# Kernel optimization log

Hardware: AMD Instinct MI355X
Metric: run time of the kernel (lower is better)

The kernel has to match this reference:

```python
import jax, jax.numpy as jnp
import numpy as np

NUM_EXPERTS = 32
TOP_K = 8
SELECT_TOP_K = 4
THRESHOLD = 0.5
HIDDEN = 2048
D_FF = 768


def setup_inputs() -> dict:
    key = jax.random.key(0)
    ks = jax.random.split(key, 5)
    hidden_states = jax.random.normal(ks[0], (4, 2048, HIDDEN), dtype=jnp.float32)
    gate_weight = jax.random.normal(ks[1], (NUM_EXPERTS, HIDDEN), dtype=jnp.float32) * 0.02
    gate_up_proj = jax.random.normal(ks[2], (NUM_EXPERTS, 2 * D_FF, HIDDEN), dtype=jnp.float32) * 0.02
    down_proj = jax.random.normal(ks[3], (NUM_EXPERTS, HIDDEN, D_FF), dtype=jnp.float32) * 0.02
    similarity = jax.random.uniform(ks[4], (NUM_EXPERTS, NUM_EXPERTS), dtype=jnp.float32)
    return {
        "hidden_states": hidden_states,
        "gate_weight": gate_weight,
        "gate_up_proj": gate_up_proj,
        "down_proj": down_proj,
        "similarity": similarity,
    }


def _moe_forward(hidden_states, gate_weight, gate_up_proj, down_proj, similarity):
    B, S_len, H = hidden_states.shape
    E, K, Ssel = NUM_EXPERTS, TOP_K, SELECT_TOP_K
    x = hidden_states.reshape(-1, H)  # [T, H]

    # Router: logits -> fp32 softmax -> top-k -> renormalize
    router_logits = x @ gate_weight.T  # [T, E]
    router_probs = jax.nn.softmax(router_logits.astype(jnp.float32), axis=-1).astype(router_logits.dtype)
    router_top_value, router_indices = jax.lax.top_k(router_probs, K)  # [T, K]
    routing_weights = router_top_value / jnp.clip(
        jnp.sum(router_top_value, axis=-1, keepdims=True), 1e-12, None
    )

    # SERE rerouting: map each secondary expert to its most-similar primary expert
    sim = similarity.astype(jnp.float32)
    sim = sim.at[jnp.arange(E), jnp.arange(E)].set(1.0)  # fill_diagonal_(1.0)
    prim = router_indices[:, :Ssel]            # [T, S]
    sec = router_indices[:, Ssel:]             # [T, K-S]
    sim_cand = sim[sec[:, :, None], prim[:, None, :]]        # [T, K-S, S]
    best_sim = jnp.max(sim_cand, axis=-1)                    # [T, K-S]
    best_i = jnp.argmax(sim_cand, axis=-1)                   # [T, K-S]
    prim_rep = jnp.broadcast_to(prim[:, None, :], sim_cand.shape)
    best_primary = jnp.take_along_axis(prim_rep, best_i[..., None], axis=-1)[..., 0]
    new_sec = jnp.where(best_sim < THRESHOLD, sec, best_primary) if THRESHOLD > 0.0 else best_primary
    rerouted_indices = jnp.concatenate([prim, new_sec], axis=1)  # [T, K]

    # Combine weights per (token, expert); duplicate expert slots accumulate (index_add semantics)
    combine = jnp.sum(
        jax.nn.one_hot(rerouted_indices, E, dtype=routing_weights.dtype)
        * routing_weights[..., None],
        axis=1,
    )  # [T, E]

    # Dense masked expert sweep (scan over experts keeps peak memory at one [T, 2*D_FF] buffer)
    def expert_step(y, params):
        wgu, wd, cw = params  # [2F, H], [H, F], [T]
        gu = x @ wgu.T                      # [T, 2F]
        g, u = jnp.split(gu, 2, axis=-1)
        h = jax.nn.silu(g) * u              # SwiGLU
        y = y + (h @ wd.T) * cw[:, None]
        return y, None

    y0 = jnp.zeros_like(x)
    y, _ = jax.lax.scan(expert_step, y0, (gate_up_proj, down_proj, combine.T))
    return y.reshape(B, S_len, H)


def reference(hidden_states, gate_weight, gate_up_proj, down_proj, similarity):
    return _moe_forward(hidden_states, gate_weight, gate_up_proj, down_proj, similarity)
```

## Files before the change

kernel.cpp:

```cpp
#include <hip/hip_runtime.h>
#include <stdint.h>
#include <string.h>

#define NTOK 8192
#define HID 2048
#define NE 32
#define DFF 768
#define NSLOT 65536
#define NB 256
#define MT 256
#define MAX_TILES 288

typedef unsigned short u16;
typedef unsigned int u32;

using f32x4 = __attribute__((ext_vector_type(4))) float;
using bf16x8 = __attribute__((ext_vector_type(8))) short;

static __device__ __forceinline__ u16 f2bf(float f) {
  u32 x = __float_as_uint(f);
  x += 0x7fffu + ((x >> 16) & 1u);
  return (u16)(x >> 16);
}

typedef const __attribute__((address_space(1))) unsigned int* gp_t;
typedef __attribute__((address_space(3))) unsigned int* lp_t;
static __device__ __forceinline__ void gload16(const void* g, void* l) {
  __builtin_amdgcn_global_load_lds((gp_t)g, (lp_t)l, 16, 0, 0);
}

__global__ void convertf2b_kernel(const float* __restrict__ src, u16* __restrict__ dst, int n4) {
  int i = blockIdx.x * blockDim.x + threadIdx.x;
  int stride = gridDim.x * blockDim.x;
  for (; i < n4; i += stride) {
    float4 v = reinterpret_cast<const float4*>(src)[i];
    u32 lo = (u32)f2bf(v.x) | ((u32)f2bf(v.y) << 16);
    u32 hi = (u32)f2bf(v.z) | ((u32)f2bf(v.w) << 16);
    reinterpret_cast<uint2*>(dst)[i] = make_uint2(lo, hi);
  }
}

__global__ void router_kernel(const float* __restrict__ x, const float* __restrict__ gw,
                              const float* __restrict__ sim,
                              int* __restrict__ slot_e, float* __restrict__ slot_w,
                              u16* __restrict__ xb) {
  int t = blockIdx.x;
  __shared__ float xs[HID];
  __shared__ float logits[NE];
  const float* xr = x + (size_t)t * HID;
  for (int i = threadIdx.x; i < HID / 4; i += 256)
    reinterpret_cast<float4*>(xs)[i] = reinterpret_cast<const float4*>(xr)[i];
  __syncthreads();
  {
    int i = threadIdx.x;
    float4 v0 = reinterpret_cast<float4*>(xs)[i * 2];
    float4 v1 = reinterpret_cast<float4*>(xs)[i * 2 + 1];
    uint4 o;
    o.x = (u32)f2bf(v0.x) | ((u32)f2bf(v0.y) << 16);
    o.y = (u32)f2bf(v0.z) | ((u32)f2bf(v0.w) << 16);
    o.z = (u32)f2bf(v1.x) | ((u32)f2bf(v1.y) << 16);
    o.w = (u32)f2bf(v1.z) | ((u32)f2bf(v1.w) << 16);
    reinterpret_cast<uint4*>(xb + (size_t)t * HID)[i] = o;
  }
  int e = threadIdx.x >> 3, part = threadIdx.x & 7;
  const float4* wv = reinterpret_cast<const float4*>(gw + (size_t)e * HID + part * 256);
  const float4* xv = reinterpret_cast<const float4*>(xs + part * 256);
  float s = 0.f;
#pragma unroll
  for (int j = 0; j < 64; ++j) {
    float4 a = xv[j], b = wv[j];
    s += a.x * b.x + a.y * b.y + a.z * b.z + a.w * b.w;
  }
  s += __shfl_xor(s, 1); s += __shfl_xor(s, 2); s += __shfl_xor(s, 4);
  if (part == 0) logits[e] = s;
  __syncthreads();
  if (threadIdx.x == 0) {
    float l[NE];
#pragma unroll
    for (int i = 0; i < NE; ++i) l[i] = logits[i];
    unsigned mask = 0;
    int idx[8]; float lv[8];
#pragma unroll
    for (int k = 0; k < 8; ++k) {
      float best = -3.4e38f; int bi = 0;
#pragma unroll
      for (int i = 0; i < NE; ++i) {
        bool ok = (((mask >> i) & 1u) == 0u) && (l[i] > best);
        best = ok ? l[i] : best;
        bi = ok ? i : bi;
      }
      idx[k] = bi; lv[k] = best; mask |= (1u << bi);
    }
    float w[8]; float ssum = 0.f;
#pragma unroll
    for (int k = 0; k < 8; ++k) { w[k] = __expf(lv[k] - lv[0]); ssum += w[k]; }
    float inv = 1.f / ssum;
    int base = t * 8;
#pragma unroll
    for (int i = 0; i < 4; ++i) { slot_e[base + i] = idx[i]; slot_w[base + i] = w[i] * inv; }
#pragma unroll
    for (int j = 0; j < 4; ++j) {
      int sj = idx[4 + j];
      float best = -2.f; int bsel = idx[0];
#pragma unroll
      for (int i = 0; i < 4; ++i) {
        int pe = idx[i];
        float sv = sim[sj * NE + pe];
        bool ok = sv > best;
        best = ok ? sv : best;
        bsel = ok ? pe : bsel;
      }
      int ns = (best < 0.5f) ? sj : bsel;
      slot_e[base + 4 + j] = ns; slot_w[base + 4 + j] = w[4 + j] * inv;
    }
  }
}

__global__ void hist_kernel(const int* __restrict__ slot_e, int* __restrict__ blockCounts) {
  __shared__ int cnt[NE];
  if (threadIdx.x < NE) cnt[threadIdx.x] = 0;
  __syncthreads();
  int i = blockIdx.x * 256 + threadIdx.x;
  atomicAdd(&cnt[slot_e[i]], 1);
  __syncthreads();
  if (threadIdx.x < NE) blockCounts[threadIdx.x * NB + blockIdx.x] = cnt[threadIdx.x];
}

__global__ void scan_kernel(const int* __restrict__ blockCounts, int* __restrict__ startEB,
                            int* __restrict__ tile_e, int* __restrict__ tile_row0,
                            int* __restrict__ tile_cnt, int* __restrict__ tileCount) {
  __shared__ int totals[NE];
  __shared__ int bases[NE];
  int t = threadIdx.x;
  if (t < NE) {
    int run = 0;
    for (int b = 0; b < NB; ++b) run += blockCounts[t * NB + b];
    totals[t] = run;
  }
  __syncthreads();
  if (t == 0) {
    int base = 0, nt = 0;
    for (int e = 0; e < NE; ++e) {
      bases[e] = base;
      int tot = totals[e];
      for (int i = 0; i < tot; i += MT) {
        tile_e[nt] = e;
        tile_row0[nt] = base + i;
        tile_cnt[nt] = (tot - i < MT) ? (tot - i) : MT;
        ++nt;
      }
      base += tot;
    }
    *tileCount = nt;
  }
  __syncthreads();
  if (t < NE) {
    int run = bases[t];
    for (int b = 0; b < NB; ++b) {
      startEB[t * NB + b] = run;
      run += blockCounts[t * NB + b];
    }
  }
}

__global__ void place_kernel(const int* __restrict__ slot_e, const float* __restrict__ slot_w,
                             const int* __restrict__ startEB,
                             int* __restrict__ perm_token, float* __restrict__ perm_w,
                             int* __restrict__ inv) {
  __shared__ int se[256];
  __shared__ float sw[256];
  int b = blockIdx.x;
  for (int i = threadIdx.x; i < 256; i += 64) {
    se[i] = slot_e[b * 256 + i];
    sw[i] = slot_w[b * 256 + i];
  }
  __syncthreads();
  int e = threadIdx.x;
  if (e < NE) {
    int pos = startEB[e * NB + b];
    for (int i = 0; i < 256; ++i) {
      if (se[i] == e) {
        perm_token[pos] = (b * 256 + i) >> 3;
        perm_w[pos] = sw[i];
        inv[b * 256 + i] = pos;
        ++pos;
      }
    }
  }
}


#define GUMM(AR, M_)                                                                   \
  acc[M_][0] = __builtin_amdgcn_mfma_f32_16x16x32_bf16(AR, b0, acc[M_][0], 0, 0, 0);   \
  acc[M_][1] = __builtin_amdgcn_mfma_f32_16x16x32_bf16(AR, b1, acc[M_][1], 0, 0, 0);   \
  acc[M_][2] = __builtin_amdgcn_mfma_f32_16x16x32_bf16(AR, b2, acc[M_][2], 0, 0, 0);   \
  acc[M_][3] = __builtin_amdgcn_mfma_f32_16x16x32_bf16(AR, b3, acc[M_][3], 0, 0, 0);

#define PH8(BUF, KK, MH, WAITK, ...)                                                   \
  do {                                                                                 \
    const u16* Ap_ = &SA[BUF][KK][abase + (MH) * 2048];                                \
    const u16* Bp_ = &SB[BUF][KK][0];                                                  \
    bf16x8 a0_ = *(const bf16x8*)(Ap_);                                                \
    bf16x8 a1_ = *(const bf16x8*)(Ap_ + 512);                                          \
    bf16x8 a2_ = *(const bf16x8*)(Ap_ + 1024);                                         \
    bf16x8 a3_ = *(const bf16x8*)(Ap_ + 1536);                                         \
    if (!(MH)) {                                                                       \
      b0 = *(const bf16x8*)(Bp_ + boff0);                                              \
      b1 = *(const bf16x8*)(Bp_ + boff1);                                              \
      b2 = *(const bf16x8*)(Bp_ + boff2);                                              \
      b3 = *(const bf16x8*)(Bp_ + boff3);                                              \
    }                                                                                  \
    __VA_ARGS__;                                                                       \
    if (WAITK) {                                                                       \
      if (tail) { asm volatile("s_waitcnt vmcnt(0)" ::: "memory"); }                   \
      else      { asm volatile("s_waitcnt vmcnt(8)" ::: "memory"); }                   \
    }                                                                                  \
    __builtin_amdgcn_s_barrier();                                                      \
    __builtin_amdgcn_s_setprio(1);                                                     \
    GUMM(a0_, (MH) * 4 + 0)                                                            \
    GUMM(a1_, (MH) * 4 + 1)                                                            \
    GUMM(a2_, (MH) * 4 + 2)                                                            \
    GUMM(a3_, (MH) * 4 + 3)                                                            \
    __builtin_amdgcn_s_setprio(0);                                                     \
    __builtin_amdgcn_sched_barrier(0);                                                 \
    __builtin_amdgcn_s_barrier();                                                      \
  } while (0)

__global__ __launch_bounds__(512, 2) void gu_fast(
    const u16* __restrict__ xb, const u16* __restrict__ wgub,
    const int* __restrict__ perm_token,
    const int* __restrict__ tile_e, const int* __restrict__ tile_row0,
    const int* __restrict__ tile_cnt, const int* __restrict__ tileCount,
    u16* __restrict__ h_perm) {
  int flat = blockIdx.x + blockIdx.y * 6;
  int xcd = flat & 7;
  int j = flat >> 3;
  int tile = xcd * 36 + j / 6;
  int n0g = (j % 6) * 128;
  if (tile >= *tileCount) return;
  int e = tile_e[tile], row0 = tile_row0[tile], cnt = tile_cnt[tile];
  __shared__ __align__(16) u16 SA[2][2][8192];
  __shared__ __align__(16) u16 SB[2][2][8192];
  __shared__ int toks[256];
  int tid = threadIdx.x;
  if (tid < 256) {
    int idx = row0 + tid;
    if (idx > NSLOT - 1) idx = NSLOT - 1;
    toks[tid] = perm_token[idx];
  }
  __syncthreads();
  int wave = tid >> 6, lane = tid & 63;
  int wr = wave >> 2, wc = wave & 3;
  int lr = lane & 15, lk = lane >> 4;
  int sr0 = tid >> 2;
  int sc0 = (tid & 3) ^ ((tid >> 3) & 3);
  const u16* gA0 = xb + (size_t)toks[sr0] * HID + sc0 * 8;
  const u16* gA1 = xb + (size_t)toks[128 + sr0] * HID + sc0 * 8;
  const u16* wgb = wgub + (size_t)e * (2 * DFF) * HID;
  const u16* gB0 = wgb + (size_t)(n0g + sr0) * HID + sc0 * 8;
  const u16* gB1 = wgb + (size_t)(DFF + n0g + sr0) * HID + sc0 * 8;
  int d0 = tid * 8, d1 = 4096 + tid * 8;

  int slot8 = (lk ^ ((lr >> 1) & 3)) * 8;
  int abase = (wr * 128 + lr) * 32 + slot8;
  int boff0 = (wc * 32 + 0 * 16 + lr) * 32 + slot8;
  int boff1 = (wc * 32 + 1 * 16 + lr) * 32 + slot8;
  int boff2 = (128 + wc * 32 + 0 * 16 + lr) * 32 + slot8;
  int boff3 = (128 + wc * 32 + 1 * 16 + lr) * 32 + slot8;

  f32x4 acc[8][4];
  f32x4 zero = {0.f, 0.f, 0.f, 0.f};
#pragma unroll
  for (int m = 0; m < 8; ++m)
#pragma unroll
    for (int n = 0; n < 4; ++n) acc[m][n] = zero;
  bf16x8 b0, b1, b2, b3;

#define GU_SGA(BUF, KK, KT) do { \
    gload16(gA0 + (KT) + (KK) * 32, &SA[BUF][KK][d0]); \
    gload16(gA1 + (KT) + (KK) * 32, &SA[BUF][KK][d1]); } while (0)
#define GU_SGB(BUF, KK, KT) do { \
    gload16(gB0 + (KT) + (KK) * 32, &SB[BUF][KK][d0]); \
    gload16(gB1 + (KT) + (KK) * 32, &SB[BUF][KK][d1]); } while (0)

  GU_SGA(0, 0, 0); GU_SGB(0, 0, 0);
  GU_SGA(0, 1, 0); GU_SGB(0, 1, 0);
  GU_SGA(1, 0, 64); GU_SGB(1, 0, 64);
  asm volatile("s_waitcnt vmcnt(8)" ::: "memory");
  __builtin_amdgcn_s_barrier();

  const int NKT = HID / 64;
  const int NI = NKT / 2;
  for (int it = 0; it < NI; ++it) {
    bool tail = (it + 2 >= NI);
    bool st = (it + 1 < NI);
    int ktA = (2 * it + 1) * 64;
    int ktB = (2 * it + 2) * 64;
    int ktC = (2 * it + 3) * 64;
    PH8(0, 0, 0, 0, GU_SGA(1, 1, ktA));
    PH8(0, 0, 1, 1, GU_SGB(1, 1, ktA));
    PH8(0, 1, 0, 0, if (st) GU_SGA(0, 0, ktB));
    PH8(0, 1, 1, 1, if (st) GU_SGB(0, 0, ktB));
    PH8(1, 0, 0, 0, if (st) GU_SGA(0, 1, ktB));
    PH8(1, 0, 1, 1, if (st) GU_SGB(0, 1, ktB));
    PH8(1, 1, 0, 0, if (st) GU_SGA(1, 0, ktC));
    PH8(1, 1, 1, 1, if (st) GU_SGB(1, 0, ktC));
  }

#pragma unroll
  for (int m = 0; m < 8; ++m)
#pragma unroll
    for (int i = 0; i < 4; ++i) {
      int row = wr * 128 + m * 16 + lk * 4 + i;
      if (row < cnt) {
#pragma unroll
        for (int nf = 0; nf < 2; ++nf) {
          int col = n0g + wc * 32 + nf * 16 + lr;
          float g = acc[m][nf][i], u = acc[m][nf + 2][i];
          float h = g / (1.f + __expf(-g)) * u;
          h_perm[(size_t)(row0 + row) * DFF + col] = f2bf(h);
        }
      }
    }
#undef GU_SGA
#undef GU_SGB
}

__global__ __launch_bounds__(512, 2) void down_fast(
    const u16* __restrict__ h_perm, const u16* __restrict__ wdb,
    const float* __restrict__ perm_w,
    const int* __restrict__ tile_e, const int* __restrict__ tile_row0,
    const int* __restrict__ tile_cnt, const int* __restrict__ tileCount,
    _Float16* __restrict__ yp) {
  int flat = blockIdx.x + blockIdx.y * 8;
  int xcd = flat & 7;
  int j = flat >> 3;
  int tile = xcd * 36 + j / 8;
  int n0 = (j % 8) * 256;
  if (tile >= *tileCount) return;
  int e = tile_e[tile], row0 = tile_row0[tile], cnt = tile_cnt[tile];
  __shared__ __align__(16) u16 SA[2][2][8192];
  __shared__ __align__(16) u16 SB[2][2][8192];
  __shared__ float wts[256];
  int tid = threadIdx.x;
  if (tid < 256) {
    int idx = row0 + tid;
    if (idx > NSLOT - 1) idx = NSLOT - 1;
    wts[tid] = perm_w[idx];
  }
  __syncthreads();
  int wave = tid >> 6, lane = tid & 63;
  int wr = wave >> 2, wc = wave & 3;
  int lr = lane & 15, lk = lane >> 4;
  int sr0 = tid >> 2;
  int sc0 = (tid & 3) ^ ((tid >> 3) & 3);
  int ia0 = row0 + sr0;       if (ia0 > NSLOT - 1) ia0 = NSLOT - 1;
  int ia1 = row0 + 128 + sr0; if (ia1 > NSLOT - 1) ia1 = NSLOT - 1;
  const u16* gA0 = h_perm + (size_t)ia0 * DFF + sc0 * 8;
  const u16* gA1 = h_perm + (size_t)ia1 * DFF + sc0 * 8;
  const u16* wb = wdb + (size_t)e * HID * DFF;
  const u16* gB0 = wb + (size_t)(n0 + sr0) * DFF + sc0 * 8;
  const u16* gB1 = wb + (size_t)(n0 + 128 + sr0) * DFF + sc0 * 8;
  int d0 = tid * 8, d1 = 4096 + tid * 8;

  int slot8 = (lk ^ ((lr >> 1) & 3)) * 8;
  int abase = (wr * 128 + lr) * 32 + slot8;
  int boff0 = (wc * 64 + 0 * 16 + lr) * 32 + slot8;
  int boff1 = (wc * 64 + 1 * 16 + lr) * 32 + slot8;
  int boff2 = (wc * 64 + 2 * 16 + lr) * 32 + slot8;
  int boff3 = (wc * 64 + 3 * 16 + lr) * 32 + slot8;

  f32x4 acc[8][4];
  f32x4 zero = {0.f, 0.f, 0.f, 0.f};
#pragma unroll
  for (int m = 0; m < 8; ++m)
#pragma unroll
    for (int n = 0; n < 4; ++n) acc[m][n] = zero;
  bf16x8 b0, b1, b2, b3;

#define DN_SGA(BUF, KK, KT) do { \
    gload16(gA0 + (KT) + (KK) * 32, &SA[BUF][KK][d0]); \
    gload16(gA1 + (KT) + (KK) * 32, &SA[BUF][KK][d1]); } while (0)
#define DN_SGB(BUF, KK, KT) do { \
    gload16(gB0 + (KT) + (KK) * 32, &SB[BUF][KK][d0]); \
    gload16(gB1 + (KT) + (KK) * 32, &SB[BUF][KK][d1]); } while (0)

  DN_SGA(0, 0, 0); DN_SGB(0, 0, 0);
  DN_SGA(0, 1, 0); DN_SGB(0, 1, 0);
  DN_SGA(1, 0, 64); DN_SGB(1, 0, 64);
  asm volatile("s_waitcnt vmcnt(8)" ::: "memory");
  __builtin_amdgcn_s_barrier();

  const int NKT = DFF / 64;
  const int NI = NKT / 2;
  for (int it = 0; it < NI; ++it) {
    bool tail = (it + 2 >= NI);
    bool st = (it + 1 < NI);
    int ktA = (2 * it + 1) * 64;
    int ktB = (2 * it + 2) * 64;
    int ktC = (2 * it + 3) * 64;
    PH8(0, 0, 0, 0, DN_SGA(1, 1, ktA));
    PH8(0, 0, 1, 1, DN_SGB(1, 1, ktA));
    PH8(0, 1, 0, 0, if (st) DN_SGA(0, 0, ktB));
    PH8(0, 1, 1, 1, if (st) DN_SGB(0, 0, ktB));
    PH8(1, 0, 0, 0, if (st) DN_SGA(0, 1, ktB));
    PH8(1, 0, 1, 1, if (st) DN_SGB(0, 1, ktB));
    PH8(1, 1, 0, 0, if (st) DN_SGA(1, 0, ktC));
    PH8(1, 1, 1, 1, if (st) DN_SGB(1, 0, ktC));
  }

#pragma unroll
  for (int m = 0; m < 8; ++m)
#pragma unroll
    for (int i = 0; i < 4; ++i) {
      int row = wr * 128 + m * 16 + lk * 4 + i;
      if (row < cnt) {
        float wt = wts[row];
#pragma unroll
        for (int nf = 0; nf < 4; ++nf) {
          int col = n0 + wc * 64 + nf * 16 + lr;
          yp[(size_t)(row0 + row) * HID + col] = (_Float16)(acc[m][nf][i] * wt);
        }
      }
    }
#undef DN_SGA
#undef DN_SGB
}

__global__ void reduce_kernel(const _Float16* __restrict__ yp, const int* __restrict__ inv,
                              float* __restrict__ y) {
  int t = blockIdx.x;
  __shared__ int pos[8];
  if (threadIdx.x < 8) pos[threadIdx.x] = inv[t * 8 + threadIdx.x];
  __syncthreads();
  int c = threadIdx.x * 8;
  float s[8] = {0.f, 0.f, 0.f, 0.f, 0.f, 0.f, 0.f, 0.f};
#pragma unroll
  for (int j = 0; j < 8; ++j) {
    uint4 v = *reinterpret_cast<const uint4*>(yp + (size_t)pos[j] * HID + c);
    const u16* p = reinterpret_cast<const u16*>(&v);
#pragma unroll
    for (int k = 0; k < 8; ++k) {
      _Float16 h;
      u16 us = p[k];
      __builtin_memcpy(&h, &us, 2);
      s[k] += (float)h;
    }
  }
  float* yo = y + (size_t)t * HID + c;
  float4 o0 = {s[0], s[1], s[2], s[3]};
  float4 o1 = {s[4], s[5], s[6], s[7]};
  *reinterpret_cast<float4*>(yo) = o0;
  *reinterpret_cast<float4*>(yo + 4) = o1;
}

extern "C" void kernel_launch(void* const* d_in, const int* in_sizes, int n_in,
                              void* d_out, int out_size, void* d_ws, size_t ws_size,
                              hipStream_t stream) {
  const float* x = (const float*)d_in[0];
  const float* gw = (const float*)d_in[1];
  const float* wgu = (const float*)d_in[2];
  const float* wd = (const float*)d_in[3];
  const float* sim = (const float*)d_in[4];
  float* y = (float*)d_out;

  char* ws = (char*)d_ws;
  size_t off = 0;
  auto alloc = [&](size_t bytes) {
    char* p = ws + off;
    off += (bytes + 255) & ~(size_t)255;
    return p;
  };
  u16* xb = (u16*)alloc((size_t)NTOK * HID * 2);
  u16* h_perm = (u16*)alloc((size_t)NSLOT * DFF * 2);
  int* slot_e = (int*)alloc(NSLOT * 4);
  float* slot_w = (float*)alloc(NSLOT * 4);
  int* perm_token = (int*)alloc(NSLOT * 4);
  float* perm_w = (float*)alloc(NSLOT * 4);
  int* inv = (int*)alloc(NSLOT * 4);
  int* blockCounts = (int*)alloc(NE * NB * 4);
  int* startEB = (int*)alloc(NE * NB * 4);
  int* tile_e = (int*)alloc(MAX_TILES * 4);
  int* tile_row0 = (int*)alloc(MAX_TILES * 4);
  int* tile_cnt = (int*)alloc(MAX_TILES * 4);
  int* tileCount = (int*)alloc(4);

  size_t wgu_elems = (size_t)NE * 2 * DFF * HID;
  size_t wd_elems = (size_t)NE * HID * DFF;
  size_t region_bytes = (size_t)NSLOT * HID * 2;
  u16* wd_b = (u16*)alloc(wd_elems * 2);
  char* region = alloc(region_bytes);
  u16* wgu_b = (u16*)region;
  _Float16* yp = (_Float16*)region;
  if (off > ws_size) return;

  router_kernel<<<NTOK, 256, 0, stream>>>(x, gw, sim, slot_e, slot_w, xb);
  hist_kernel<<<NB, 256, 0, stream>>>(slot_e, blockCounts);
  scan_kernel<<<1, 64, 0, stream>>>(blockCounts, startEB, tile_e, tile_row0, tile_cnt, tileCount);
  place_kernel<<<NB, 64, 0, stream>>>(slot_e, slot_w, startEB, perm_token, perm_w, inv);

  convertf2b_kernel<<<4096, 256, 0, stream>>>(wgu, wgu_b, (int)(wgu_elems / 4));
  convertf2b_kernel<<<4096, 256, 0, stream>>>(wd, wd_b, (int)(wd_elems / 4));
  gu_fast<<<dim3(DFF / 128, MAX_TILES), 512, 0, stream>>>(
      xb, wgu_b, perm_token, tile_e, tile_row0, tile_cnt, tileCount, h_perm);
  down_fast<<<dim3(HID / 256, MAX_TILES), 512, 0, stream>>>(
      h_perm, wd_b, perm_w, tile_e, tile_row0, tile_cnt, tileCount, yp);
  reduce_kernel<<<NTOK, 256, 0, stream>>>(yp, inv, y);
}
```

Before: 1.222 ms.

## Restructure GEMM main loop to one barrier per k-window with peeled tail

Replaces the eight-phase loop, which had two barriers per phase, with a four-window schedule. Each window waits on LDS and global counters, issues a single barrier, then runs both M-halves of MFMAs with the global prefetches placed between them. The last iteration is peeled so the in-loop stage/tail conditionals disappear and vmcnt waits are static. The aim is to cut barrier and synchronisation overhead in both the gate-up and down kernels, at the cost of a riskier cross-buffer reuse ordering that now depends on a single barrier.

After: 1.194 ms. 1.02x faster.

```diff
diff --git a/kernel.cpp b/kernel.cpp
--- a/kernel.cpp
+++ b/kernel.cpp
@@ -196,34 +196,34 @@
   acc[M_][2] = __builtin_amdgcn_mfma_f32_16x16x32_bf16(AR, b2, acc[M_][2], 0, 0, 0);   \
   acc[M_][3] = __builtin_amdgcn_mfma_f32_16x16x32_bf16(AR, b3, acc[M_][3], 0, 0, 0);
 
-#define PH8(BUF, KK, MH, WAITK, ...)                                                   \
+#define GWIN(BUF, KK, VM, S1, S2)                                                      \
   do {                                                                                 \
-    const u16* Ap_ = &SA[BUF][KK][abase + (MH) * 2048];                                \
+    asm volatile("s_waitcnt lgkmcnt(0)" ::: "memory");                                 \
+    __builtin_amdgcn_sched_barrier(0);                                                 \
+    asm volatile("s_waitcnt vmcnt(" #VM ")" ::: "memory");                             \
+    __builtin_amdgcn_s_barrier();                                                      \
+    const u16* Ap_ = &SA[BUF][KK][abase];                                              \
     const u16* Bp_ = &SB[BUF][KK][0];                                                  \
     bf16x8 a0_ = *(const bf16x8*)(Ap_);                                                \
     bf16x8 a1_ = *(const bf16x8*)(Ap_ + 512);                                          \
     bf16x8 a2_ = *(const bf16x8*)(Ap_ + 1024);                                         \
     bf16x8 a3_ = *(const bf16x8*)(Ap_ + 1536);                                         \
-    if (!(MH)) {                                                                       \
-      b0 = *(const bf16x8*)(Bp_ + boff0);                                              \
-      b1 = *(const bf16x8*)(Bp_ + boff1);                                              \
-      b2 = *(const bf16x8*)(Bp_ + boff2);                                              \
-      b3 = *(const bf16x8*)(Bp_ + boff3);                                              \
-    }                                                                                  \
-    __VA_ARGS__;                                                                       \
-    if (WAITK) {                                                                       \
-      if (tail) { asm volatile("s_waitcnt vmcnt(0)" ::: "memory"); }                   \
-      else      { asm volatile("s_waitcnt vmcnt(8)" ::: "memory"); }                   \
-    }                                                                                  \
-    __builtin_amdgcn_s_barrier();                                                      \
+    bf16x8 b0 = *(const bf16x8*)(Bp_ + boff0);                                         \
+    bf16x8 b1 = *(const bf16x8*)(Bp_ + boff1);                                         \
+    bf16x8 b2 = *(const bf16x8*)(Bp_ + boff2);                                         \
+    bf16x8 b3 = *(const bf16x8*)(Bp_ + boff3);                                         \
+    S1;                                                                                \
     __builtin_amdgcn_s_setprio(1);                                                     \
-    GUMM(a0_, (MH) * 4 + 0)                                                            \
-    GUMM(a1_, (MH) * 4 + 1)                                                            \
-    GUMM(a2_, (MH) * 4 + 2)                                                            \
-    GUMM(a3_, (MH) * 4 + 3)                                                            \
+    GUMM(a0_, 0) GUMM(a1_, 1) GUMM(a2_, 2) GUMM(a3_, 3)                                \
     __builtin_amdgcn_s_setprio(0);                                                     \
-    __builtin_amdgcn_sched_barrier(0);                                                 \
-    __builtin_amdgcn_s_barrier();                                                      \
+    bf16x8 c0_ = *(const bf16x8*)(Ap_ + 2048);                                         \
+    bf16x8 c1_ = *(const bf16x8*)(Ap_ + 2560);                                         \
+    bf16x8 c2_ = *(const bf16x8*)(Ap_ + 3072);                                         \
+    bf16x8 c3_ = *(const bf16x8*)(Ap_ + 3584);                                         \
+    S2;                                                                                \
+    __builtin_amdgcn_s_setprio(1);                                                     \
+    GUMM(c0_, 4) GUMM(c1_, 5) GUMM(c2_, 6) GUMM(c3_, 7)                                \
+    __builtin_amdgcn_s_setprio(0);                                                     \
   } while (0)
 
 __global__ __launch_bounds__(512, 2) void gu_fast(
@@ -274,7 +274,6 @@
   for (int m = 0; m < 8; ++m)
 #pragma unroll
     for (int n = 0; n < 4; ++n) acc[m][n] = zero;
-  bf16x8 b0, b1, b2, b3;
 
 #define GU_SGA(BUF, KK, KT) do { \
     gload16(gA0 + (KT) + (KK) * 32, &SA[BUF][KK][d0]); \
@@ -286,25 +285,24 @@
   GU_SGA(0, 0, 0); GU_SGB(0, 0, 0);
   GU_SGA(0, 1, 0); GU_SGB(0, 1, 0);
   GU_SGA(1, 0, 64); GU_SGB(1, 0, 64);
-  asm volatile("s_waitcnt vmcnt(8)" ::: "memory");
-  __builtin_amdgcn_s_barrier();
 
   const int NKT = HID / 64;
   const int NI = NKT / 2;
-  for (int it = 0; it < NI; ++it) {
-    bool tail = (it + 2 >= NI);
-    bool st = (it + 1 < NI);
+  for (int it = 0; it < NI - 1; ++it) {
     int ktA = (2 * it + 1) * 64;
     int ktB = (2 * it + 2) * 64;
     int ktC = (2 * it + 3) * 64;
-    PH8(0, 0, 0, 0, GU_SGA(1, 1, ktA));
-    PH8(0, 0, 1, 1, GU_SGB(1, 1, ktA));
-    PH8(0, 1, 0, 0, if (st) GU_SGA(0, 0, ktB));
-    PH8(0, 1, 1, 1, if (st) GU_SGB(0, 0, ktB));
-    PH8(1, 0, 0, 0, if (st) GU_SGA(0, 1, ktB));
-    PH8(1, 0, 1, 1, if (st) GU_SGB(0, 1, ktB));
-    PH8(1, 1, 0, 0, if (st) GU_SGA(1, 0, ktC));
-    PH8(1, 1, 1, 1, if (st) GU_SGB(1, 0, ktC));
+    GWIN(0, 0, 8, GU_SGA(1, 1, ktA), GU_SGB(1, 1, ktA));
+    GWIN(0, 1, 8, GU_SGA(0, 0, ktB), GU_SGB(0, 0, ktB));
+    GWIN(1, 0, 8, GU_SGA(0, 1, ktB), GU_SGB(0, 1, ktB));
+    GWIN(1, 1, 8, GU_SGA(1, 0, ktC), GU_SGB(1, 0, ktC));
+  }
+  {
+    int ktA = (2 * (NI - 1) + 1) * 64;
+    GWIN(0, 0, 8, GU_SGA(1, 1, ktA), GU_SGB(1, 1, ktA));
+    GWIN(0, 1, 8, (void)0, (void)0);
+    GWIN(1, 0, 4, (void)0, (void)0);
+    GWIN(1, 1, 0, (void)0, (void)0);
   }
 
 #pragma unroll
@@ -376,7 +374,6 @@
   for (int m = 0; m < 8; ++m)
 #pragma unroll
     for (int n = 0; n < 4; ++n) acc[m][n] = zero;
-  bf16x8 b0, b1, b2, b3;
 
 #define DN_SGA(BUF, KK, KT) do { \
     gload16(gA0 + (KT) + (KK) * 32, &SA[BUF][KK][d0]); \
@@ -388,25 +385,24 @@
   DN_SGA(0, 0, 0); DN_SGB(0, 0, 0);
   DN_SGA(0, 1, 0); DN_SGB(0, 1, 0);
   DN_SGA(1, 0, 64); DN_SGB(1, 0, 64);
-  asm volatile("s_waitcnt vmcnt(8)" ::: "memory");
-  __builtin_amdgcn_s_barrier();
 
   const int NKT = DFF / 64;
   const int NI = NKT / 2;
-  for (int it = 0; it < NI; ++it) {
-    bool tail = (it + 2 >= NI);
-    bool st = (it + 1 < NI);
+  for (int it = 0; it < NI - 1; ++it) {
     int ktA = (2 * it + 1) * 64;
     int ktB = (2 * it + 2) * 64;
     int ktC = (2 * it + 3) * 64;
-    PH8(0, 0, 0, 0, DN_SGA(1, 1, ktA));
-    PH8(0, 0, 1, 1, DN_SGB(1, 1, ktA));
-    PH8(0, 1, 0, 0, if (st) DN_SGA(0, 0, ktB));
-    PH8(0, 1, 1, 1, if (st) DN_SGB(0, 0, ktB));
-    PH8(1, 0, 0, 0, if (st) DN_SGA(0, 1, ktB));
-    PH8(1, 0, 1, 1, if (st) DN_SGB(0, 1, ktB));
-    PH8(1, 1, 0, 0, if (st) DN_SGA(1, 0, ktC));
-    PH8(1, 1, 1, 1, if (st) DN_SGB(1, 0, ktC));
+    GWIN(0, 0, 8, DN_SGA(1, 1, ktA), DN_SGB(1, 1, ktA));
+    GWIN(0, 1, 8, DN_SGA(0, 0, ktB), DN_SGB(0, 0, ktB));
+    GWIN(1, 0, 8, DN_SGA(0, 1, ktB), DN_SGB(0, 1, ktB));
+    GWIN(1, 1, 8, DN_SGA(1, 0, ktC), DN_SGB(1, 0, ktC));
+  }
+  {
+    int ktA = (2 * (NI - 1) + 1) * 64;
+    GWIN(0, 0, 8, DN_SGA(1, 1, ktA), DN_SGB(1, 1, ktA));
+    GWIN(0, 1, 8, (void)0, (void)0);
+    GWIN(1, 0, 4, (void)0, (void)0);
+    GWIN(1, 1, 0, (void)0, (void)0);
   }
 
 #pragma unroll
```
